# Optimization experiments

Hardware: AMD Instinct MI355X
Metric: run time of the kernel (lower is better)

The kernel has to match this reference:

```python
import jax, jax.numpy as jnp
import numpy as np

NINP, NHID, NOUT = 400, 600, 400
HS = NHID + NOUT          # h_size = nhid + nout
NLEVELS, K, AUX_FREQ = 40, 2, 20
DILATION = [1]


def setup_inputs() -> dict:
    key = jax.random.key(0)
    ks = jax.random.split(key, 6)
    B, T = 8, 256
    bound = 0.01  # matches init_weights normal_(0, 0.01)
    return {
        "X": jax.random.normal(ks[0], (B, NINP, T), jnp.float32),
        "hid": jax.random.normal(ks[1], (B, HS, 1), jnp.float32),
        "cell": jax.random.normal(ks[2], (B, HS, 1), jnp.float32),
        "w1": jax.random.normal(ks[3], (4 * HS, NINP, K), jnp.float32) * bound,
        "w2": jax.random.normal(ks[4], (4 * HS, HS, K), jnp.float32) * bound,
        "b2": jax.random.normal(ks[5], (4 * HS,), jnp.float32) * bound,
    }


def _conv1d(x, w, d):
    # x: [B, Cin, T_padded], w: [Cout, Cin, K] -> [B, Cout, T]
    return jax.lax.conv_general_dilated(
        x, w, window_strides=(1,), padding='VALID', rhs_dilation=(d,),
        dimension_numbers=('NCH', 'OIH', 'NCH'))


def _forward(X, hid, cell, w1, w2, b2):
    B, _, T = X.shape
    ht = jnp.zeros((B, HS, T), X.dtype)
    ct = jnp.zeros((B, HS, T), X.dtype)

    # Input-side convolution is weight-tied and X never changes across levels,
    # so (like the torch dict cache) compute it once per distinct dilation.
    conv1 = {}
    for d in set(DILATION):
        pad = (K - 1) * d
        xp = jnp.pad(X, ((0, 0), (0, 0), (pad, 0)))
        conv1[d] = _conv1d(xp, w1, d)

    aux = []
    for i in range(NLEVELS):
        d = DILATION[i % len(DILATION)]
        pad = (K - 1) * d
        # causal left-pad of the hidden stream, filled with the initial hid
        z1 = jnp.concatenate([jnp.broadcast_to(hid, (B, HS, pad)), ht], axis=2)
        out = conv1[d] + _conv1d(z1, w2, d) + b2[None, :, None]  # [B, 4*HS, T]
        # shifted cell state, first d steps filled with the initial cell
        ct_1 = jnp.concatenate(
            [jnp.broadcast_to(cell, (B, HS, d)), ct[:, :, :-d]], axis=2)
        it = jax.nn.sigmoid(out[:, :HS])
        ot = jax.nn.sigmoid(out[:, HS:2 * HS])
        gt = jnp.tanh(out[:, 2 * HS:3 * HS])
        ft = jax.nn.sigmoid(out[:, 3 * HS:])
        ct = ft * ct_1 + it * gt
        ht = ot * jnp.tanh(ct)
        if i % AUX_FREQ == AUX_FREQ - 1:
            aux.append(ht[:, -NOUT:])  # [B, nout, T]

    out_main = jnp.transpose(ht[:, -NOUT:], (0, 2, 1))            # [B, T, nout]
    hc = (ht[:, :, -1:], ct[:, :, -1:])                            # ([B,HS,1], [B,HS,1])
    aux_outs = jnp.transpose(jnp.stack(aux, axis=0), (1, 0, 3, 2))  # [B, n_aux, T, nout]
    return out_main, hc, aux_outs


def reference(X, hid, cell, w1, w2, b2):
    return _forward(X, hid, cell, w1, w2, b2)
```

## Files before the change

kernel.cpp:

```cpp
#include <hip/hip_runtime.h>
#include <hip/hip_bf16.h>
#include <math.h>

typedef __bf16 bf16;
typedef __bf16 bf16x8 __attribute__((ext_vector_type(8)));
typedef __bf16 bf16x4 __attribute__((ext_vector_type(4)));
typedef float f32x4 __attribute__((ext_vector_type(4)));
typedef unsigned int u32;
typedef u32 u32x4 __attribute__((ext_vector_type(4)));

#define NINP 400
#define HS   1000
#define HP   1024
#define B_   8
#define T_   256
#define NT   2048
#define K2   2048
#define K1   1024
#define M_   4096

#define HT_OFF   819200
#define CT_OFF   827200
#define AUX_OFF  835200

typedef __attribute__((address_space(1))) const void gvoid;
typedef __attribute__((address_space(3))) void lvoid;

__device__ __forceinline__ void async_copy16(void* lds, const void* g) {
  __builtin_amdgcn_global_load_lds((gvoid*)g, (lvoid*)lds, 16, 0, 0);
}

__device__ __forceinline__ float sigm(float x) { return 1.0f / (1.0f + expf(-x)); }


__global__ void repack_w1(const float* __restrict__ w1, bf16* __restrict__ W1q) {
  int idx = blockIdx.x * 256 + threadIdx.x;
  if (idx >= M_ * K1) return;
  int pm = idx >> 10, k = idx & 1023;
  int g = (pm >> 4) & 3;
  int h = (pm >> 7) * 32 + ((pm >> 6) & 1) * 16 + (pm & 15);
  float v = 0.0f;
  if (h < HS) {
    int c = g * HS + h;
    if (k < 512) { if (k < NINP) v = w1[(size_t)c * (NINP * 2) + k * 2 + 0]; }
    else { int j = k - 512; if (j < NINP) v = w1[(size_t)c * (NINP * 2) + j * 2 + 1]; }
  }
  W1q[idx] = (bf16)v;
}

__global__ void repack_w2(const float* __restrict__ w2, bf16* __restrict__ W2q) {
  int idx = blockIdx.x * 256 + threadIdx.x;
  if (idx >= M_ * K2) return;
  int pm = idx >> 11, k = idx & 2047;
  int g = (pm >> 4) & 3;
  int h = (pm >> 7) * 32 + ((pm >> 6) & 1) * 16 + (pm & 15);
  float v = 0.0f;
  if (h < HS) {
    int c = g * HS + h;
    if (k < HP) { if (k < HS) v = w2[(size_t)c * (HS * 2) + k * 2 + 0]; }
    else { int j = k - HP; if (j < HS) v = w2[(size_t)c * (HS * 2) + j * 2 + 1]; }
  }
  W2q[idx] = (bf16)v;
}

__global__ void build_xt(const float* __restrict__ X, bf16* __restrict__ XT) {
  int idx = blockIdx.x * 256 + threadIdx.x;
  if (idx >= NT * K1) return;
  int n = idx >> 10, k = idx & 1023;
  int b = n >> 8, t = n & (T_ - 1);
  float v = 0.0f;
  if (k < 512) { if (k < NINP && t > 0) v = X[((size_t)b * NINP + k) * T_ + t - 1]; }
  else { int j = k - 512; if (j < NINP) v = X[((size_t)b * NINP + j) * T_ + t]; }
  XT[idx] = (bf16)v;
}

__global__ void build_hc(const float* __restrict__ hid, const float* __restrict__ cell,
                         bf16* __restrict__ hidp, float* __restrict__ cellp) {
  int idx = blockIdx.x * 256 + threadIdx.x;
  if (idx >= B_ * HP) return;
  int b = idx >> 10, k = idx & (HP - 1);
  hidp[idx]  = (k < HS) ? (bf16)hid[b * HS + k] : (bf16)0.0f;
  cellp[idx] = (k < HS) ? cell[b * HS + k] : 0.0f;
}


template <bool GATED>
__global__ __launch_bounds__(256, 2) void gemm_step(
    const bf16* __restrict__ A,
    const bf16* __restrict__ Bsrc,
    const bf16* __restrict__ hidp,
    const bf16* __restrict__ CbIn,
    bf16* __restrict__ CbOut,
    const float* __restrict__ b2,
    const bf16* __restrict__ ctprev,
    const float* __restrict__ cellp,
    bf16* __restrict__ ctnew,
    bf16* __restrict__ Hnew,
    int K) {
  __shared__ bf16 SMEM[2][128][64];

  const int tid = threadIdx.x;
  const int lane = tid & 63;
  const int w = tid >> 6;
  const int mh = w >> 1, nh = w & 1;
  const int dr = lane >> 3, c8 = lane & 7;
  const int swo = ((c8 - dr) & 7) * 8;
  const int quad = lane >> 4, col = lane & 15;

  int n0, bm;
  if (GATED) {
    const int L = blockIdx.y * gridDim.x + blockIdx.x;
    bm = (L & 7) * 4 + (L >> 7);
    n0 = ((L >> 3) & 15) * 128;
  } else {
    n0 = blockIdx.x * 128;
    bm = blockIdx.y;
  }

  f32x4 acc[4][4];
#pragma unroll
  for (int i = 0; i < 4; ++i)
#pragma unroll
    for (int j = 0; j < 4; ++j) acc[i][j] = (f32x4){0.f, 0.f, 0.f, 0.f};

  const int NIT = K >> 6;
  for (int it = 0; it < NIT; ++it) {
    const int k0 = it << 6;
    __syncthreads();
#pragma unroll
    for (int inst = 0; inst < 4; ++inst) {
      const int r = inst * 32 + w * 8 + dr;
      async_copy16(&SMEM[0][inst * 32 + w * 8][0],
                   A + (size_t)(bm * 128 + r) * K + k0 + swo);
      const int n = n0 + r;
      const bf16* bp;
      if (GATED) {
        const int kk = (k0 & (HP - 1)) + swo;
        if (k0 < HP) {
          const int t = n & (T_ - 1);
          bp = (t == 0) ? (hidp + (size_t)(n >> 8) * HP + kk)
                        : (Bsrc + (size_t)(n - 1) * HP + kk);
        } else {
          bp = Bsrc + (size_t)n * HP + kk;
        }
      } else {
        bp = Bsrc + (size_t)n * K + k0 + swo;
      }
      async_copy16(&SMEM[1][inst * 32 + w * 8][0], bp);
    }
    __syncthreads();
#pragma unroll
    for (int kc = 0; kc < 64; kc += 32) {
      bf16x8 av[4], bv[4];
#pragma unroll
      for (int mt = 0; mt < 4; ++mt) {
        const int rA = mh * 64 + mt * 16 + col;
        av[mt] = *(const bf16x8*)&SMEM[0][rA][(((kc >> 3) + quad + rA) & 7) * 8];
      }
#pragma unroll
      for (int nt = 0; nt < 4; ++nt) {
        const int rB = nh * 64 + nt * 16 + col;
        bv[nt] = *(const bf16x8*)&SMEM[1][rB][(((kc >> 3) + quad + rB) & 7) * 8];
      }
#pragma unroll
      for (int mt = 0; mt < 4; ++mt)
#pragma unroll
        for (int nt = 0; nt < 4; ++nt)
          acc[mt][nt] = __builtin_amdgcn_mfma_f32_16x16x32_bf16(av[mt], bv[nt], acc[mt][nt], 0, 0, 0);
    }
  }

  if (!GATED) {
    __syncthreads();
    bf16 (*Csh)[128] = (bf16(*)[128])&SMEM[0][0][0];
#pragma unroll
    for (int mt = 0; mt < 4; ++mt) {
#pragma unroll
      for (int nt = 0; nt < 4; ++nt) {
        const int nloc = nh * 64 + nt * 16 + col;
        bf16x4 v;
#pragma unroll
        for (int j = 0; j < 4; ++j) {
          const int h = bm * 32 + mh * 16 + quad * 4 + j;
          const float bias = (h < HS) ? b2[mt * HS + h] : 0.0f;
          v[j] = (bf16)(acc[mt][nt][j] + bias);
        }
        *(bf16x4*)&Csh[nloc][mh * 64 + mt * 16 + quad * 4] = v;
      }
    }
    __syncthreads();
#pragma unroll
    for (int i2 = 0; i2 < 8; ++i2) {
      const int idx = i2 * 256 + tid;
      const int rrow = idx >> 4, off = idx & 15;
      *(u32x4*)&CbOut[(size_t)(n0 + rrow) * 4096 + bm * 128 + off * 8] =
          *(const u32x4*)&Csh[rrow][off * 8];
    }
  } else {
    __syncthreads();
    bf16 (*Hsh)[32] = (bf16(*)[32])&SMEM[0][0][0];
#pragma unroll
    for (int nt = 0; nt < 4; ++nt) {
      const int nloc = nh * 64 + nt * 16 + col;
      const int n = n0 + nloc;
      const int b = n >> 8;
      const int t = n & (T_ - 1);
      const size_t cb = (size_t)n * 4096 + (size_t)(bm * 2 + mh) * 64 + quad * 4;
      bf16x4 c0 = *(const bf16x4*)&CbIn[cb + 0];
      bf16x4 c1 = *(const bf16x4*)&CbIn[cb + 16];
      bf16x4 c2 = *(const bf16x4*)&CbIn[cb + 32];
      bf16x4 c3 = *(const bf16x4*)&CbIn[cb + 48];
      bf16x4 hv;
#pragma unroll
      for (int j = 0; j < 4; ++j) {
        const int h = bm * 32 + mh * 16 + quad * 4 + j;
        const float ci = acc[0][nt][j] + (float)c0[j];
        const float co = acc[1][nt][j] + (float)c1[j];
        const float cg = acc[2][nt][j] + (float)c2[j];
        const float cf = acc[3][nt][j] + (float)c3[j];
        const float ctold = (t == 0) ? cellp[b * HP + h]
                                     : (float)ctprev[(size_t)h * NT + (n - 1)];
        const float cn = sigm(cf) * ctold + sigm(ci) * tanhf(cg);
        ctnew[(size_t)h * NT + n] = (bf16)cn;
        hv[j] = (bf16)(sigm(co) * tanhf(cn));
      }
      *(bf16x4*)&Hsh[nloc][mh * 16 + quad * 4] = hv;
    }
    __syncthreads();
#pragma unroll
    for (int i2 = 0; i2 < 2; ++i2) {
      const int idx = i2 * 256 + tid;
      const int rrow = idx >> 2, off = idx & 3;
      *(u32x4*)&Hnew[(size_t)(n0 + rrow) * HP + bm * 32 + off * 8] =
          *(const u32x4*)&Hsh[rrow][off * 8];
    }
  }
}


__global__ void aux_kernel(const bf16* __restrict__ H, float* __restrict__ out, int s) {
  int idx = blockIdx.x * 256 + threadIdx.x;
  if (idx >= NT * 100) return;
  int n = idx / 100;
  int o = (idx % 100) * 4;
  int b = n >> 8, t = n & (T_ - 1);
  bf16x4 v = *(const bf16x4*)&H[(size_t)n * HP + 600 + o];
  f32x4 f = {(float)v[0], (float)v[1], (float)v[2], (float)v[3]};
  *(f32x4*)&out[AUX_OFF + ((size_t)((b * 2 + s) * T_ + t)) * 400 + o] = f;
}

__global__ void final_kernel(const bf16* __restrict__ H, const bf16* __restrict__ ct,
                             float* __restrict__ out) {
  int idx = blockIdx.x * 256 + threadIdx.x;
  if (idx < NT * 100) {
    int n = idx / 100;
    int o = (idx % 100) * 4;
    int b = n >> 8, t = n & (T_ - 1);
    bf16x4 v = *(const bf16x4*)&H[(size_t)n * HP + 600 + o];
    f32x4 f = {(float)v[0], (float)v[1], (float)v[2], (float)v[3]};
    *(f32x4*)&out[(size_t)n * 400 + o] = f;
    *(f32x4*)&out[AUX_OFF + ((size_t)((b * 2 + 1) * T_ + t)) * 400 + o] = f;
  } else {
    int j = idx - NT * 100;
    if (j < 8000) {
      int b = j / 1000, h = j % 1000;
      out[HT_OFF + j] = (float)H[(size_t)(b * T_ + 255) * HP + h];
    } else if (j < 16000) {
      int jj = j - 8000;
      int b = jj / 1000, h = jj % 1000;
      out[CT_OFF + jj] = (float)ct[(size_t)h * NT + b * T_ + 255];
    }
  }
}


extern "C" void kernel_launch(void* const* d_in, const int* in_sizes, int n_in,
                              void* d_out, int out_size, void* d_ws, size_t ws_size,
                              hipStream_t stream) {
  const float* X    = (const float*)d_in[0];
  const float* hid  = (const float*)d_in[1];
  const float* cell = (const float*)d_in[2];
  const float* w1   = (const float*)d_in[3];
  const float* w2   = (const float*)d_in[4];
  const float* b2   = (const float*)d_in[5];
  float* out = (float*)d_out;

  char* ws = (char*)d_ws;
  size_t off = 0;
  auto alloc = [&](size_t bytes) {
    void* p = ws + off;
    off += (bytes + 255) & ~(size_t)255;
    return p;
  };
  bf16* W2q    = (bf16*)alloc((size_t)M_ * K2 * 2);
  bf16* CbP    = (bf16*)alloc((size_t)NT * M_ * 2);
  bf16* Hb0    = (bf16*)alloc((size_t)NT * HP * 2);
  bf16* ctb0   = (bf16*)alloc((size_t)HP * NT * 2);
  bf16* hidp   = (bf16*)alloc((size_t)B_ * HP * 2);
  float* cellp = (float*)alloc((size_t)B_ * HP * 4);
  char* R = (char*)alloc((size_t)12 * 1024 * 1024);
  bf16* W1q  = (bf16*)R;
  bf16* XT   = (bf16*)(R + (size_t)8 * 1024 * 1024);
  bf16* ctb1 = (bf16*)R;
  bf16* Hb1  = (bf16*)(R + (size_t)4 * 1024 * 1024);

  bf16* Hb[2]  = {Hb0, Hb1};
  bf16* ctb[2] = {ctb0, ctb1};

  hipMemsetAsync(Hb[0], 0, (size_t)NT * HP * 2, stream);
  hipMemsetAsync(ctb[0], 0, (size_t)HP * NT * 2, stream);

  repack_w1<<<(M_ * K1) / 256, 256, 0, stream>>>(w1, W1q);
  repack_w2<<<(M_ * K2) / 256, 256, 0, stream>>>(w2, W2q);
  build_xt<<<(NT * K1) / 256, 256, 0, stream>>>(X, XT);
  build_hc<<<(B_ * HP) / 256, 256, 0, stream>>>(hid, cell, hidp, cellp);

  dim3 grid(NT / 128, M_ / 128);
  gemm_step<false><<<grid, 256, 0, stream>>>(W1q, XT, nullptr, nullptr, CbP, b2,
                                             nullptr, nullptr, nullptr, nullptr, K1);
  for (int i = 0; i < 40; ++i) {
    int p = i & 1;
    gemm_step<true><<<grid, 256, 0, stream>>>(W2q, Hb[p], hidp, CbP, nullptr, nullptr,
                                              ctb[p], cellp, ctb[p ^ 1], Hb[p ^ 1], K2);
    if (i == 19) aux_kernel<<<800, 256, 0, stream>>>(Hb[p ^ 1], out, 0);
  }
  final_kernel<<<(NT * 100 + 16000 + 255) / 256, 256, 0, stream>>>(Hb[0], ctb[0], out);
}
```

Measured before the change: 2.001 ms.

## Use 256x128 tiles with 8 waves, double-buffered LDS and early Cb prefetch

```diff
diff --git a/kernel.cpp b/kernel.cpp
--- a/kernel.cpp
+++ b/kernel.cpp
@@ -85,7 +85,7 @@
 
 
 template <bool GATED>
-__global__ __launch_bounds__(256, 2) void gemm_step(
+__global__ __launch_bounds__(512, 2) void gemm_step(
     const bf16* __restrict__ A,
     const bf16* __restrict__ Bsrc,
     const bf16* __restrict__ hidp,
@@ -97,24 +97,33 @@
     bf16* __restrict__ ctnew,
     bf16* __restrict__ Hnew,
     int K) {
-  __shared__ bf16 SMEM[2][128][64];
+  __shared__ bf16 As[2][256][64];
+  __shared__ bf16 Bs[2][128][64];
 
   const int tid = threadIdx.x;
   const int lane = tid & 63;
   const int w = tid >> 6;
-  const int mh = w >> 1, nh = w & 1;
+  const int mh = w >> 1;
+  const int nh = w & 1;
   const int dr = lane >> 3, c8 = lane & 7;
   const int swo = ((c8 - dr) & 7) * 8;
   const int quad = lane >> 4, col = lane & 15;
 
-  int n0, bm;
+  const int L = blockIdx.y * 16 + blockIdx.x;
+  const int bm = (L & 7) * 2 + (L >> 7);
+  const int n0 = ((L >> 3) & 15) * 128;
+
+  bf16x4 cb0[4], cb1[4], cb2[4], cb3[4];
   if (GATED) {
-    const int L = blockIdx.y * gridDim.x + blockIdx.x;
-    bm = (L & 7) * 4 + (L >> 7);
-    n0 = ((L >> 3) & 15) * 128;
-  } else {
-    n0 = blockIdx.x * 128;
-    bm = blockIdx.y;
+#pragma unroll
+    for (int nt = 0; nt < 4; ++nt) {
+      const int n = n0 + nh * 64 + nt * 16 + col;
+      const size_t cb = (size_t)n * 4096 + (size_t)(bm * 256 + mh * 64) + quad * 4;
+      cb0[nt] = *(const bf16x4*)&CbIn[cb + 0];
+      cb1[nt] = *(const bf16x4*)&CbIn[cb + 16];
+      cb2[nt] = *(const bf16x4*)&CbIn[cb + 32];
+      cb3[nt] = *(const bf16x4*)&CbIn[cb + 48];
+    }
   }
 
   f32x4 acc[4][4];
@@ -123,15 +132,16 @@
 #pragma unroll
     for (int j = 0; j < 4; ++j) acc[i][j] = (f32x4){0.f, 0.f, 0.f, 0.f};
 
-  const int NIT = K >> 6;
-  for (int it = 0; it < NIT; ++it) {
-    const int k0 = it << 6;
-    __syncthreads();
-#pragma unroll
-    for (int inst = 0; inst < 4; ++inst) {
-      const int r = inst * 32 + w * 8 + dr;
-      async_copy16(&SMEM[0][inst * 32 + w * 8][0],
-                   A + (size_t)(bm * 128 + r) * K + k0 + swo);
+  auto stage = [&](int buf, int k0) {
+#pragma unroll
+    for (int i = 0; i < 4; ++i) {
+      const int r = i * 64 + w * 8 + dr;
+      async_copy16(&As[buf][i * 64 + w * 8][0],
+                   A + (size_t)(bm * 256 + r) * K + k0 + swo);
+    }
+#pragma unroll
+    for (int j = 0; j < 2; ++j) {
+      const int r = j * 64 + w * 8 + dr;
       const int n = n0 + r;
       const bf16* bp;
       if (GATED) {
@@ -146,33 +156,42 @@
       } else {
         bp = Bsrc + (size_t)n * K + k0 + swo;
       }
-      async_copy16(&SMEM[1][inst * 32 + w * 8][0], bp);
-    }
-    __syncthreads();
+      async_copy16(&Bs[buf][j * 64 + w * 8][0], bp);
+    }
+  };
+
+  const int NIT = K >> 6;
+  stage(0, 0);
+  __syncthreads();
+  for (int it = 0; it < NIT; ++it) {
+    const int cur = it & 1;
+    if (it + 1 < NIT) stage(cur ^ 1, (it + 1) << 6);
 #pragma unroll
     for (int kc = 0; kc < 64; kc += 32) {
       bf16x8 av[4], bv[4];
 #pragma unroll
       for (int mt = 0; mt < 4; ++mt) {
         const int rA = mh * 64 + mt * 16 + col;
-        av[mt] = *(const bf16x8*)&SMEM[0][rA][(((kc >> 3) + quad + rA) & 7) * 8];
+        av[mt] = *(const bf16x8*)&As[cur][rA][(((kc >> 3) + quad + rA) & 7) * 8];
       }
 #pragma unroll
       for (int nt = 0; nt < 4; ++nt) {
         const int rB = nh * 64 + nt * 16 + col;
-        bv[nt] = *(const bf16x8*)&SMEM[1][rB][(((kc >> 3) + quad + rB) & 7) * 8];
-      }
+        bv[nt] = *(const bf16x8*)&Bs[cur][rB][(((kc >> 3) + quad + rB) & 7) * 8];
+      }
+      __builtin_amdgcn_s_setprio(1);
 #pragma unroll
       for (int mt = 0; mt < 4; ++mt)
 #pragma unroll
         for (int nt = 0; nt < 4; ++nt)
           acc[mt][nt] = __builtin_amdgcn_mfma_f32_16x16x32_bf16(av[mt], bv[nt], acc[mt][nt], 0, 0, 0);
-    }
+      __builtin_amdgcn_s_setprio(0);
+    }
+    __syncthreads();
   }
 
   if (!GATED) {
-    __syncthreads();
-    bf16 (*Csh)[128] = (bf16(*)[128])&SMEM[0][0][0];
+    bf16 (*Csh)[256] = (bf16(*)[256])&As[0][0][0];
 #pragma unroll
     for (int mt = 0; mt < 4; ++mt) {
 #pragma unroll
@@ -181,7 +200,7 @@
         bf16x4 v;
 #pragma unroll
         for (int j = 0; j < 4; ++j) {
-          const int h = bm * 32 + mh * 16 + quad * 4 + j;
+          const int h = bm * 64 + mh * 16 + quad * 4 + j;
           const float bias = (h < HS) ? b2[mt * HS + h] : 0.0f;
           v[j] = (bf16)(acc[mt][nt][j] + bias);
         }
@@ -191,33 +210,27 @@
     __syncthreads();
 #pragma unroll
     for (int i2 = 0; i2 < 8; ++i2) {
-      const int idx = i2 * 256 + tid;
-      const int rrow = idx >> 4, off = idx & 15;
-      *(u32x4*)&CbOut[(size_t)(n0 + rrow) * 4096 + bm * 128 + off * 8] =
+      const int idx = i2 * 512 + tid;
+      const int rrow = idx >> 5, off = idx & 31;
+      *(u32x4*)&CbOut[(size_t)(n0 + rrow) * 4096 + bm * 256 + off * 8] =
           *(const u32x4*)&Csh[rrow][off * 8];
     }
   } else {
-    __syncthreads();
-    bf16 (*Hsh)[32] = (bf16(*)[32])&SMEM[0][0][0];
+    bf16 (*Hsh)[64] = (bf16(*)[64])&As[0][0][0];
 #pragma unroll
     for (int nt = 0; nt < 4; ++nt) {
       const int nloc = nh * 64 + nt * 16 + col;
       const int n = n0 + nloc;
       const int b = n >> 8;
       const int t = n & (T_ - 1);
-      const size_t cb = (size_t)n * 4096 + (size_t)(bm * 2 + mh) * 64 + quad * 4;
-      bf16x4 c0 = *(const bf16x4*)&CbIn[cb + 0];
-      bf16x4 c1 = *(const bf16x4*)&CbIn[cb + 16];
-      bf16x4 c2 = *(const bf16x4*)&CbIn[cb + 32];
-      bf16x4 c3 = *(const bf16x4*)&CbIn[cb + 48];
       bf16x4 hv;
 #pragma unroll
       for (int j = 0; j < 4; ++j) {
-        const int h = bm * 32 + mh * 16 + quad * 4 + j;
-        const float ci = acc[0][nt][j] + (float)c0[j];
-        const float co = acc[1][nt][j] + (float)c1[j];
-        const float cg = acc[2][nt][j] + (float)c2[j];
-        const float cf = acc[3][nt][j] + (float)c3[j];
+        const int h = bm * 64 + mh * 16 + quad * 4 + j;
+        const float ci = acc[0][nt][j] + (float)cb0[nt][j];
+        const float co = acc[1][nt][j] + (float)cb1[nt][j];
+        const float cg = acc[2][nt][j] + (float)cb2[nt][j];
+        const float cf = acc[3][nt][j] + (float)cb3[nt][j];
         const float ctold = (t == 0) ? cellp[b * HP + h]
                                      : (float)ctprev[(size_t)h * NT + (n - 1)];
         const float cn = sigm(cf) * ctold + sigm(ci) * tanhf(cg);
@@ -229,9 +242,9 @@
     __syncthreads();
 #pragma unroll
     for (int i2 = 0; i2 < 2; ++i2) {
-      const int idx = i2 * 256 + tid;
-      const int rrow = idx >> 2, off = idx & 3;
-      *(u32x4*)&Hnew[(size_t)(n0 + rrow) * HP + bm * 32 + off * 8] =
+      const int idx = i2 * 512 + tid;
+      const int rrow = idx >> 3, off = idx & 7;
+      *(u32x4*)&Hnew[(size_t)(n0 + rrow) * HP + bm * 64 + off * 8] =
           *(const u32x4*)&Hsh[rrow][off * 8];
     }
   }
@@ -315,12 +328,12 @@
   build_xt<<<(NT * K1) / 256, 256, 0, stream>>>(X, XT);
   build_hc<<<(B_ * HP) / 256, 256, 0, stream>>>(hid, cell, hidp, cellp);
 
-  dim3 grid(NT / 128, M_ / 128);
-  gemm_step<false><<<grid, 256, 0, stream>>>(W1q, XT, nullptr, nullptr, CbP, b2,
+  dim3 grid(16, 16);
+  gemm_step<false><<<grid, 512, 0, stream>>>(W1q, XT, nullptr, nullptr, CbP, b2,
                                              nullptr, nullptr, nullptr, nullptr, K1);
   for (int i = 0; i < 40; ++i) {
     int p = i & 1;
-    gemm_step<true><<<grid, 256, 0, stream>>>(W2q, Hb[p], hidp, CbP, nullptr, nullptr,
+    gemm_step<true><<<grid, 512, 0, stream>>>(W2q, Hb[p], hidp, CbP, nullptr, nullptr,
                                               ctb[p], cellp, ctb[p ^ 1], Hb[p ^ 1], K2);
     if (i == 19) aux_kernel<<<800, 256, 0, stream>>>(Hb[p ^ 1], out, 0);
   }
```

Result: slower. 2.340 ms (+16.9%).
